# Kernel tuning notes

Hardware: AMD Instinct MI355X
Metric: run time of the kernel (lower is better)

Reference implementation:

```python
import jax, jax.numpy as jnp
import numpy as np

EPS = 1e-5

def _temporal_conv(x_bcnt, w, b):
    # x: (B,C,N,T), w: (O,I,1,K), pad time dim by K//2
    k = w.shape[-1]
    y = jax.lax.conv_general_dilated(
        x_bcnt, w, window_strides=(1, 1),
        padding=[(0, 0), (k // 2, k // 2)],
        dimension_numbers=("NCHW", "OIHW", "NCHW"))
    return y + b[None, :, None, None]

def _gcn(x_btnc, edge_index, w, b):
    # GCNConv: add self-loops, symmetric normalization, linear, scatter-add, bias.
    B, T, N, C = x_btnc.shape
    src = jnp.concatenate([edge_index[0], jnp.arange(N)])
    dst = jnp.concatenate([edge_index[1], jnp.arange(N)])
    ew = jnp.ones(src.shape[0], dtype=x_btnc.dtype)
    deg = jax.ops.segment_sum(ew, dst, num_segments=N)
    dinv = jnp.where(deg > 0, jax.lax.rsqrt(jnp.maximum(deg, 1e-12)), 0.0)
    norm = dinv[src] * dinv[dst] * ew  # (E+N,)
    xh = jnp.einsum("btnc,cd->btnd", x_btnc, w)
    msgs = xh[:, :, src, :] * norm[None, None, :, None]  # (B,T,E+N,C)
    agg = jnp.zeros_like(xh).at[:, :, dst, :].add(msgs)
    return agg + b

def _batchnorm2d(x_bcnt, gamma, beta):
    mean = jnp.mean(x_bcnt, axis=(0, 2, 3), keepdims=True)
    var = jnp.mean((x_bcnt - mean) ** 2, axis=(0, 2, 3), keepdims=True)
    xn = (x_bcnt - mean) * jax.lax.rsqrt(var + EPS)
    return xn * gamma[None, :, None, None] + beta[None, :, None, None]

def setup_inputs() -> dict:
    key = jax.random.key(0)
    ks = jax.random.split(key, 10)
    B, T, N, C = 1, 64, 2000, 64
    E, K = 32000, 3
    s = 1.0 / np.sqrt(C * K)
    inp = {
        "x": jax.random.normal(ks[0], (B, T, N, C), dtype=jnp.float32),
        "edge_index": jax.random.randint(ks[1], (2, E), 0, N, dtype=jnp.int64),
        "conv1_w": jax.random.uniform(ks[2], (C, C, 1, K), jnp.float32, -s, s),
        "conv1_b": jax.random.uniform(ks[3], (C,), jnp.float32, -s, s),
        "gcn_w": jax.random.normal(ks[4], (C, C), dtype=jnp.float32) / np.sqrt(C),
        "gcn_b": jnp.zeros((C,), dtype=jnp.float32),
        "conv2_w": jax.random.uniform(ks[5], (C, C, 1, K), jnp.float32, -s, s),
        "conv2_b": jax.random.uniform(ks[6], (C,), jnp.float32, -s, s),
        "bn_gamma": jnp.ones((C,), dtype=jnp.float32),
        "bn_beta": jnp.zeros((C,), dtype=jnp.float32),
    }
    return inp

def reference(x, edge_index, conv1_w, conv1_b, gcn_w, gcn_b, conv2_w, conv2_b, bn_gamma, bn_beta):
    # x: (B,T,N,C) -> (B,C,N,T)
    h = jnp.transpose(x, (0, 3, 2, 1))
    h = _temporal_conv(h, conv1_w, conv1_b)
    h = jnp.transpose(h, (0, 3, 2, 1))  # (B,T,N,C)
    h = _gcn(h, edge_index, gcn_w, gcn_b)
    h = jnp.transpose(h, (0, 3, 2, 1))  # (B,C,N,T)
    h = _temporal_conv(h, conv2_w, conv2_b)
    h = _batchnorm2d(h, bn_gamma, bn_beta)
    h = jax.nn.relu(h)
    return jnp.transpose(h, (0, 3, 2, 1))  # (B,T,N,C)
```

## Files before the change

kernel.cpp:

```cpp
#include <hip/hip_runtime.h>

#define T_DIM 64
#define N_DIM 2000
#define C_DIM 64
#define E_DIM 32000
#define ROWS (T_DIM * N_DIM)
#define BN_EPS 1e-5f
#define TCHUNK 4
#define UPN 2

typedef short s8v __attribute__((ext_vector_type(8)));
typedef float f4v __attribute__((ext_vector_type(4)));

__device__ __forceinline__ ushort f2b(float f) {
    unsigned u = __float_as_uint(f);
    unsigned r = u + 0x7FFF + ((u >> 16) & 1);
    return (ushort)(r >> 16);
}
__device__ __forceinline__ float b2f(ushort h) {
    return __uint_as_float(((unsigned)h) << 16);
}
__device__ __forceinline__ s8v pack8(float4 a, float4 b) {
    s8v r;
    r[0] = (short)f2b(a.x); r[1] = (short)f2b(a.y);
    r[2] = (short)f2b(a.z); r[3] = (short)f2b(a.w);
    r[4] = (short)f2b(b.x); r[5] = (short)f2b(b.y);
    r[6] = (short)f2b(b.z); r[7] = (short)f2b(b.w);
    return r;
}

__global__ void k_degscan(const int* __restrict__ ei, int* __restrict__ offs,
                          float* __restrict__ dinv, int* __restrict__ cursor,
                          int2* __restrict__ edat, float* __restrict__ bnstats) {
    __shared__ int a[2048], b[2048];
    int tid = threadIdx.x;
    for (int i = tid; i < 2048; i += 1024) a[i] = 0;
    __syncthreads();
    for (int e = tid; e < E_DIM; e += 1024) atomicAdd(&a[ei[E_DIM + e]], 1);
    __syncthreads();
    for (int i = tid; i < 2048; i += 1024) a[i] = (i < N_DIM) ? (a[i] + 1) : 0;
    __syncthreads();
    int* s = a; int* d = b;
    for (int off = 1; off < 2048; off <<= 1) {
        for (int i = tid; i < 2048; i += 1024)
            d[i] = s[i] + ((i >= off) ? s[i - off] : 0);
        __syncthreads();
        int* t = s; s = d; d = t;
    }
    for (int i = tid; i < 2048; i += 1024)
        if (i <= N_DIM) offs[i] = (i == 0) ? 0 : s[i - 1];
    for (int n = tid; n < N_DIM; n += 1024) {
        int pre = (n == 0) ? 0 : s[n - 1];
        int dp1 = s[n] - pre;
        float dn = rsqrtf((float)dp1);
        dinv[n] = dn;
        edat[pre] = make_int2(n, __float_as_int(dn * dn));
        cursor[n] = 1;
    }
    if (tid < 128) bnstats[tid] = 0.f;
}

__global__ __launch_bounds__(256) void k_fillw(
    const int* __restrict__ ei, const int* __restrict__ offs,
    const float* __restrict__ dinv, int* __restrict__ cursor,
    int2* __restrict__ edat,
    const float* __restrict__ c1w, const float* __restrict__ c1b,
    const float* __restrict__ gw, const float* __restrict__ gb,
    const float* __restrict__ c2b, const float* __restrict__ c2w,
    ushort* __restrict__ W5f, ushort* __restrict__ Wc,
    float* __restrict__ bz, float* __restrict__ beta) {
    int tid = threadIdx.x;
    if (blockIdx.x < 125) {
        int e = blockIdx.x * 256 + tid;
        if (e < E_DIM) {
            int s = ei[e];
            int d = ei[E_DIM + e];
            int p = atomicAdd(&cursor[d], 1);
            edat[offs[d] + p] = make_int2(s, __float_as_int(dinv[s] * dinv[d]));
        }
        return;
    }
    __shared__ float Gl[3][64];
    __shared__ float b1l[64], gbl[64];
    int i = blockIdx.x - 125;
    if (tid < 192) {
        int j = tid >> 6, c = tid & 63;
        float s = 0.f;
        for (int o = 0; o < 64; ++o)
            s += c1w[o * 192 + i * 3 + j] * gw[o * 64 + c];
        Gl[j][c] = s;
    } else {
        int c = tid - 192;
        float s = 0.f;
        if (i == 0)
            for (int o = 0; o < 64; ++o) s += c1b[o] * gw[o * 64 + c];
        b1l[c] = s;
        gbl[c] = gb[c];
    }
    __syncthreads();
    if (tid < 64) {
        int n = tid;
        float d00 = 0.f, d01 = 0.f, d02 = 0.f;
        float d10 = 0.f, d11 = 0.f, d12 = 0.f;
        float d20 = 0.f, d21 = 0.f, d22 = 0.f;
        for (int c = 0; c < 64; ++c) {
            float a0 = Gl[0][c], a1 = Gl[1][c], a2 = Gl[2][c];
            float b0 = c2w[n * 192 + c * 3 + 0];
            float b1 = c2w[n * 192 + c * 3 + 1];
            float b2 = c2w[n * 192 + c * 3 + 2];
            d00 += a0 * b0; d01 += a0 * b1; d02 += a0 * b2;
            d10 += a1 * b0; d11 += a1 * b1; d12 += a1 * b2;
            d20 += a2 * b0; d21 += a2 * b1; d22 += a2 * b2;
        }
        float wm[5];
        wm[0] = d00;
        wm[1] = d01 + d10;
        wm[2] = d02 + d11 + d20;
        wm[3] = d12 + d21;
        wm[4] = d22;
        for (int m = 0; m < 5; ++m) {
            int kk = m * 64 + i;
            int flat = (((kk >> 5) * 4 + (n >> 4)) * 64 + ((kk >> 3) & 3) * 16 + (n & 15)) * 8 + (kk & 7);
            W5f[flat] = f2b(wm[m]);
        }
        int fc = (((i >> 5) * 4 + (n >> 4)) * 64 + ((i >> 3) & 3) * 16 + (n & 15)) * 8 + (i & 7);
        Wc[fc] = f2b(-d20);
        Wc[4096 + fc] = f2b(-d02);
        if (i == 0) {
            float s1[3] = {0.f, 0.f, 0.f}, s2[3] = {0.f, 0.f, 0.f};
            for (int k = 0; k < 3; ++k)
                for (int c = 0; c < 64; ++c) {
                    float w2 = c2w[n * 192 + c * 3 + k];
                    s1[k] += b1l[c] * w2;
                    s2[k] += gbl[c] * w2;
                }
            bz[n]        = s1[0] + s1[1] + s1[2];
            bz[64 + n]   = s1[1] + s1[2];
            bz[128 + n]  = s1[0] + s1[1];
            float cb = c2b[n];
            beta[n]       = s2[0] + s2[1] + s2[2] + cb;
            beta[64 + n]  = s2[1] + s2[2] + cb;
            beta[128 + n] = s2[0] + s2[1] + cb;
        }
    }
}

__global__ __launch_bounds__(256) void k_conv5(
    const float* __restrict__ x, const ushort* __restrict__ W5f,
    const ushort* __restrict__ Wcg, const float* __restrict__ bz,
    ushort* __restrict__ z) {
    __shared__ __align__(16) ushort Wl[20480];
    __shared__ __align__(16) ushort Cl[4096];
    __shared__ __align__(16) ushort Eb[4][1280];

    int tid = threadIdx.x, wv = tid >> 6, lane = tid & 63;
    int ml = lane & 15, q = lane >> 4;
    int n0 = blockIdx.x * 64;
    int t0 = blockIdx.y * TCHUNK;
    int n = n0 + wv * 16 + ml;
    bool nok = (n < N_DIM);
    const float* xrow = x + (size_t)n * 64 + q * 8;

    #pragma unroll
    for (int o = 0; o < 10; ++o) {
        int idx = tid + o * 256;
        *(s8v*)&Wl[idx * 8] = *(const s8v*)&W5f[idx * 8];
    }
    bool bnd0 = (t0 == 0), bnd1 = (t0 + TCHUNK == T_DIM);
    if (bnd0 || bnd1) {
        const ushort* src = Wcg + (bnd1 ? 4096 : 0);
        #pragma unroll
        for (int o = 0; o < 2; ++o) {
            int idx = tid + o * 256;
            *(s8v*)&Cl[idx * 8] = *(const s8v*)&src[idx * 8];
        }
    }

    const s8v ZV = {0, 0, 0, 0, 0, 0, 0, 0};
    s8v a[16];
    #pragma unroll
    for (int i = 0; i < 16; ++i) a[i] = ZV;

    #pragma unroll
    for (int i = 0; i < 5; ++i) {
        int s = t0 - 2 + i;
        if (nok && s >= 0 && s < T_DIM) {
            const float* p = xrow + (size_t)s * N_DIM * 64;
            float4 v0 = *(const float4*)p;
            float4 v1 = *(const float4*)(p + 4);
            float4 v2 = *(const float4*)(p + 32);
            float4 v3 = *(const float4*)(p + 36);
            a[2 * i]     = pack8(v0, v1);
            a[2 * i + 1] = pack8(v2, v3);
        }
    }
    __syncthreads();

    #pragma unroll
    for (int p = 0; p < TCHUNK; ++p) {
        int t = t0 + p;
        float4 r0, r1, r2, r3;
        bool pf = false;
        if (p < TCHUNK - 1) {
            int s = t0 + 3 + p;
            if (nok && s < T_DIM) {
                pf = true;
                const float* pp = xrow + (size_t)s * N_DIM * 64;
                r0 = *(const float4*)pp;
                r1 = *(const float4*)(pp + 4);
                r2 = *(const float4*)(pp + 32);
                r3 = *(const float4*)(pp + 36);
            }
        }

        f4v acc[4];
        #pragma unroll
        for (int c = 0; c < 4; ++c) acc[c] = (f4v){0.f, 0.f, 0.f, 0.f};

        #pragma unroll
        for (int sg = 0; sg < 10; ++sg) {
            #pragma unroll
            for (int c = 0; c < 4; ++c) {
                s8v bf = *(const s8v*)&Wl[((sg * 4 + c) * 64 + lane) * 8];
                acc[c] = __builtin_amdgcn_mfma_f32_16x16x32_bf16(a[2 * p + sg], bf, acc[c], 0, 0, 0);
            }
        }
        if (bnd0 && p == 0) {
            #pragma unroll
            for (int s2 = 0; s2 < 2; ++s2)
                #pragma unroll
                for (int c = 0; c < 4; ++c) {
                    s8v bf = *(const s8v*)&Cl[((s2 * 4 + c) * 64 + lane) * 8];
                    acc[c] = __builtin_amdgcn_mfma_f32_16x16x32_bf16(a[4 + s2], bf, acc[c], 0, 0, 0);
                }
        }
        if (bnd1 && p == TCHUNK - 1) {
            #pragma unroll
            for (int s2 = 0; s2 < 2; ++s2)
                #pragma unroll
                for (int c = 0; c < 4; ++c) {
                    s8v bf = *(const s8v*)&Cl[((s2 * 4 + c) * 64 + lane) * 8];
                    acc[c] = __builtin_amdgcn_mfma_f32_16x16x32_bf16(a[10 + s2], bf, acc[c], 0, 0, 0);
                }
        }

        int cls = (bnd0 && p == 0) ? 1 : ((bnd1 && p == TCHUNK - 1) ? 2 : 0);
        ushort* eb = &Eb[wv][0];
        #pragma unroll
        for (int c = 0; c < 4; ++c) {
            int col = c * 16 + ml;
            float bb = bz[cls * 64 + col];
            #pragma unroll
            for (int rg = 0; rg < 4; ++rg)
                eb[(q * 4 + rg) * 80 + col] = f2b(acc[c][rg] + bb);
        }
        int rr = lane >> 2, cof = (lane & 3) * 16;
        int gn = n0 + wv * 16 + rr;
        if (gn < N_DIM) {
            ushort* dst = &z[((size_t)t * N_DIM + gn) * 64 + cof];
            *(s8v*)dst       = *(const s8v*)&eb[rr * 80 + cof];
            *(s8v*)(dst + 8) = *(const s8v*)&eb[rr * 80 + cof + 8];
        }
        if (p < TCHUNK - 1) {
            a[10 + 2 * p] = pf ? pack8(r0, r1) : ZV;
            a[11 + 2 * p] = pf ? pack8(r2, r3) : ZV;
        }
    }
}

__global__ __launch_bounds__(256) void k_gather(
    const ushort* __restrict__ zb, const int* __restrict__ offs,
    const int2* __restrict__ edat, const float* __restrict__ beta,
    ushort* __restrict__ yb, float* __restrict__ bnstats) {
    __shared__ float ssum[64], ssq[64];
    int tid = threadIdx.x;
    if (tid < 64) { ssum[tid] = 0.f; ssq[tid] = 0.f; }
    __syncthreads();

    int tg = blockIdx.x;
    int nb = blockIdx.y;
    int wv = tid >> 6, lane = tid & 63;
    int u = lane >> 3;
    int c8 = (lane & 7) * 8;
    int t = tg * 8 + u;
    int cls = (t == 0) ? 1 : ((t == 63) ? 2 : 0);
    const float* bp = beta + cls * 64 + c8;
    float4 b0 = *(const float4*)bp;
    float4 b1 = *(const float4*)(bp + 4);
    float bb[8] = {b0.x, b0.y, b0.z, b0.w, b1.x, b1.y, b1.z, b1.w};
    const ushort* zl = zb + (size_t)t * (N_DIM * 64) + c8;

    float sr[8] = {0.f,0.f,0.f,0.f,0.f,0.f,0.f,0.f};
    float qr[8] = {0.f,0.f,0.f,0.f,0.f,0.f,0.f,0.f};

    #pragma unroll
    for (int nn = 0; nn < UPN; ++nn) {
        int n = nb * (4 * UPN) + wv * UPN + nn;
        int beg = offs[n], end = offs[n + 1];

        float acc[8] = {0.f,0.f,0.f,0.f,0.f,0.f,0.f,0.f};
        int j = beg;
        for (; j + 1 < end; j += 2) {
            int2 e0 = edat[j];
            int2 e1 = edat[j + 1];
            float w0 = __int_as_float(e0.y);
            float w1 = __int_as_float(e1.y);
            s8v v0 = *(const s8v*)(zl + (size_t)e0.x * 64);
            s8v v1 = *(const s8v*)(zl + (size_t)e1.x * 64);
            #pragma unroll
            for (int i = 0; i < 8; ++i) acc[i] += w0 * b2f((ushort)v0[i]);
            #pragma unroll
            for (int i = 0; i < 8; ++i) acc[i] += w1 * b2f((ushort)v1[i]);
        }
        if (j < end) {
            int2 e0 = edat[j];
            float w0 = __int_as_float(e0.y);
            s8v v0 = *(const s8v*)(zl + (size_t)e0.x * 64);
            #pragma unroll
            for (int i = 0; i < 8; ++i) acc[i] += w0 * b2f((ushort)v0[i]);
        }

        s8v pk;
        #pragma unroll
        for (int i = 0; i < 8; ++i) {
            float y = acc[i] + bb[i];
            pk[i] = (short)f2b(y);
            sr[i] += y;
            qr[i] += y * y;
        }
        *(s8v*)&yb[((size_t)t * N_DIM + n) * 64 + c8] = pk;
    }

    #pragma unroll
    for (int dd = 8; dd <= 32; dd <<= 1)
        #pragma unroll
        for (int i = 0; i < 8; ++i) {
            sr[i] += __shfl_xor(sr[i], dd);
            qr[i] += __shfl_xor(qr[i], dd);
        }
    if (u == 0) {
        #pragma unroll
        for (int i = 0; i < 8; ++i) {
            atomicAdd(&ssum[c8 + i], sr[i]);
            atomicAdd(&ssq[c8 + i], qr[i]);
        }
    }
    __syncthreads();
    if (tid < 64) {
        atomicAdd(&bnstats[tid], ssum[tid]);
        atomicAdd(&bnstats[64 + tid], ssq[tid]);
    }
}

__global__ __launch_bounds__(256) void k_bn(const ushort* __restrict__ yb,
                                            const float* __restrict__ bnstats,
                                            const float* __restrict__ gamma,
                                            const float* __restrict__ beta,
                                            float* __restrict__ out) {
    __shared__ float sscale[64], sshift[64];
    int tid = threadIdx.x;
    if (tid < 64) {
        float m = bnstats[tid] * (1.0f / ROWS);
        float v = bnstats[64 + tid] * (1.0f / ROWS) - m * m;
        float sc = gamma[tid] * rsqrtf(v + BN_EPS);
        sscale[tid] = sc;
        sshift[tid] = beta[tid] - m * sc;
    }
    __syncthreads();
    const int total8 = ROWS * 8;
    for (int i8 = blockIdx.x * 256 + tid; i8 < total8; i8 += gridDim.x * 256) {
        s8v v = *(const s8v*)&yb[(size_t)i8 * 8];
        int c8 = (i8 & 7) * 8;
        f4v o0, o1;
        o0[0] = fmaxf(b2f((ushort)v[0]) * sscale[c8 + 0] + sshift[c8 + 0], 0.f);
        o0[1] = fmaxf(b2f((ushort)v[1]) * sscale[c8 + 1] + sshift[c8 + 1], 0.f);
        o0[2] = fmaxf(b2f((ushort)v[2]) * sscale[c8 + 2] + sshift[c8 + 2], 0.f);
        o0[3] = fmaxf(b2f((ushort)v[3]) * sscale[c8 + 3] + sshift[c8 + 3], 0.f);
        o1[0] = fmaxf(b2f((ushort)v[4]) * sscale[c8 + 4] + sshift[c8 + 4], 0.f);
        o1[1] = fmaxf(b2f((ushort)v[5]) * sscale[c8 + 5] + sshift[c8 + 5], 0.f);
        o1[2] = fmaxf(b2f((ushort)v[6]) * sscale[c8 + 6] + sshift[c8 + 6], 0.f);
        o1[3] = fmaxf(b2f((ushort)v[7]) * sscale[c8 + 7] + sshift[c8 + 7], 0.f);
        __builtin_nontemporal_store(o0, (f4v*)&out[(size_t)i8 * 8]);
        __builtin_nontemporal_store(o1, (f4v*)&out[(size_t)i8 * 8 + 4]);
    }
}

extern "C" void kernel_launch(void* const* d_in, const int* in_sizes, int n_in,
                              void* d_out, int out_size, void* d_ws, size_t ws_size,
                              hipStream_t stream) {
    const float* x   = (const float*)d_in[0];
    const int*   ei  = (const int*)d_in[1];
    const float* c1w = (const float*)d_in[2];
    const float* c1b = (const float*)d_in[3];
    const float* gw  = (const float*)d_in[4];
    const float* gb  = (const float*)d_in[5];
    const float* c2w = (const float*)d_in[6];
    const float* c2b = (const float*)d_in[7];
    const float* bng = (const float*)d_in[8];
    const float* bnb = (const float*)d_in[9];
    float* out = (float*)d_out;

    ushort* yb     = (ushort*)d_ws;
    ushort* W5f    = yb + (size_t)ROWS * 64;
    ushort* Wc     = W5f + 20480;
    float*  bz     = (float*)(Wc + 8192);
    float*  beta   = bz + 192;
    float*  dinv   = beta + 192;
    float*  bnstats= dinv + 2000;
    int*    offs   = (int*)(bnstats + 128);
    int*    cursor = offs + 2001;
    int2*   edat   = (int2*)((char*)(cursor + 2000) +
                     (((size_t)(cursor + 2000)) % 8 ? 4 : 0));

    ushort* zb = (ushort*)d_out;

    k_degscan<<<1, 1024, 0, stream>>>(ei, offs, dinv, cursor, edat, bnstats);
    k_fillw<<<189, 256, 0, stream>>>(ei, offs, dinv, cursor, edat,
                                     c1w, c1b, gw, gb, c2b, c2w, W5f, Wc, bz, beta);
    k_conv5<<<dim3(32, T_DIM / TCHUNK), 256, 0, stream>>>(x, W5f, Wc, bz, zb);
    k_gather<<<dim3(8, 250), 256, 0, stream>>>(zb, offs, edat, beta, yb, bnstats);
    k_bn<<<2048, 256, 0, stream>>>(yb, bnstats, bng, bnb, out);
}
```

Measured before the change: 211.7 us.

## Stage gather edge lists in LDS and unroll neighbor loads by eight

```diff
diff --git a/kernel.cpp b/kernel.cpp
--- a/kernel.cpp
+++ b/kernel.cpp
@@ -7,7 +7,7 @@
 #define ROWS (T_DIM * N_DIM)
 #define BN_EPS 1e-5f
 #define TCHUNK 4
-#define UPN 2
+#define GEMAX 1024
 
 typedef short s8v __attribute__((ext_vector_type(8)));
 typedef float f4v __attribute__((ext_vector_type(4)));
@@ -268,17 +268,28 @@
     }
 }
 
-__global__ __launch_bounds__(256) void k_gather(
+__global__ __launch_bounds__(512) void k_gather(
     const ushort* __restrict__ zb, const int* __restrict__ offs,
     const int2* __restrict__ edat, const float* __restrict__ beta,
     ushort* __restrict__ yb, float* __restrict__ bnstats) {
     __shared__ float ssum[64], ssq[64];
+    __shared__ int2 eLds[GEMAX];
+    __shared__ int eoff[9];
     int tid = threadIdx.x;
     if (tid < 64) { ssum[tid] = 0.f; ssq[tid] = 0.f; }
-    __syncthreads();
 
     int tg = blockIdx.x;
     int nb = blockIdx.y;
+    int n0 = nb * 8;
+    if (tid < 9) eoff[tid] = offs[n0 + tid];
+    __syncthreads();
+    int ebase = eoff[0];
+    int ecnt = eoff[8] - ebase;
+    bool inLds = (ecnt <= GEMAX);
+    if (inLds)
+        for (int i = tid; i < ecnt; i += 512) eLds[i] = edat[ebase + i];
+    __syncthreads();
+
     int wv = tid >> 6, lane = tid & 63;
     int u = lane >> 3;
     int c8 = (lane & 7) * 8;
@@ -290,46 +301,52 @@
     float bb[8] = {b0.x, b0.y, b0.z, b0.w, b1.x, b1.y, b1.z, b1.w};
     const ushort* zl = zb + (size_t)t * (N_DIM * 64) + c8;
 
-    float sr[8] = {0.f,0.f,0.f,0.f,0.f,0.f,0.f,0.f};
-    float qr[8] = {0.f,0.f,0.f,0.f,0.f,0.f,0.f,0.f};
-
-    #pragma unroll
-    for (int nn = 0; nn < UPN; ++nn) {
-        int n = nb * (4 * UPN) + wv * UPN + nn;
-        int beg = offs[n], end = offs[n + 1];
-
-        float acc[8] = {0.f,0.f,0.f,0.f,0.f,0.f,0.f,0.f};
-        int j = beg;
-        for (; j + 1 < end; j += 2) {
-            int2 e0 = edat[j];
-            int2 e1 = edat[j + 1];
-            float w0 = __int_as_float(e0.y);
-            float w1 = __int_as_float(e1.y);
-            s8v v0 = *(const s8v*)(zl + (size_t)e0.x * 64);
-            s8v v1 = *(const s8v*)(zl + (size_t)e1.x * 64);
-            #pragma unroll
-            for (int i = 0; i < 8; ++i) acc[i] += w0 * b2f((ushort)v0[i]);
-            #pragma unroll
-            for (int i = 0; i < 8; ++i) acc[i] += w1 * b2f((ushort)v1[i]);
-        }
-        if (j < end) {
-            int2 e0 = edat[j];
-            float w0 = __int_as_float(e0.y);
-            s8v v0 = *(const s8v*)(zl + (size_t)e0.x * 64);
-            #pragma unroll
-            for (int i = 0; i < 8; ++i) acc[i] += w0 * b2f((ushort)v0[i]);
-        }
-
-        s8v pk;
-        #pragma unroll
-        for (int i = 0; i < 8; ++i) {
-            float y = acc[i] + bb[i];
-            pk[i] = (short)f2b(y);
-            sr[i] += y;
-            qr[i] += y * y;
-        }
-        *(s8v*)&yb[((size_t)t * N_DIM + n) * 64 + c8] = pk;
-    }
+    int n = n0 + wv;
+    int beg = eoff[wv] - ebase;
+    int len = eoff[wv + 1] - ebase - beg;
+
+    float acc[8] = {0.f,0.f,0.f,0.f,0.f,0.f,0.f,0.f};
+
+    if (inLds) {
+        for (int k = 0; k < len; k += 8) {
+            int2 e[8];
+            #pragma unroll
+            for (int i = 0; i < 8; ++i) {
+                int kk = k + i;
+                e[i] = eLds[beg + (kk < len ? kk : 0)];
+            }
+            s8v v[8];
+            #pragma unroll
+            for (int i = 0; i < 8; ++i)
+                v[i] = *(const s8v*)(zl + (size_t)e[i].x * 64);
+            #pragma unroll
+            for (int i = 0; i < 8; ++i) {
+                float w = (k + i < len) ? __int_as_float(e[i].y) : 0.f;
+                #pragma unroll
+                for (int j = 0; j < 8; ++j) acc[j] += w * b2f((ushort)v[i][j]);
+            }
+        }
+    } else {
+        const int2* eg = edat + ebase;
+        for (int k = 0; k < len; ++k) {
+            int2 e = eg[beg + k];
+            float w = __int_as_float(e.y);
+            s8v v = *(const s8v*)(zl + (size_t)e.x * 64);
+            #pragma unroll
+            for (int i = 0; i < 8; ++i) acc[i] += w * b2f((ushort)v[i]);
+        }
+    }
+
+    float sr[8], qr[8];
+    s8v pk;
+    #pragma unroll
+    for (int i = 0; i < 8; ++i) {
+        float y = acc[i] + bb[i];
+        pk[i] = (short)f2b(y);
+        sr[i] = y;
+        qr[i] = y * y;
+    }
+    *(s8v*)&yb[((size_t)t * N_DIM + n) * 64 + c8] = pk;
 
     #pragma unroll
     for (int dd = 8; dd <= 32; dd <<= 1)
@@ -418,6 +435,6 @@
     k_fillw<<<189, 256, 0, stream>>>(ei, offs, dinv, cursor, edat,
                                      c1w, c1b, gw, gb, c2b, c2w, W5f, Wc, bz, beta);
     k_conv5<<<dim3(32, T_DIM / TCHUNK), 256, 0, stream>>>(x, W5f, Wc, bz, zb);
-    k_gather<<<dim3(8, 250), 256, 0, stream>>>(zb, offs, edat, beta, yb, bnstats);
+    k_gather<<<dim3(8, 250), 512, 0, stream>>>(zb, offs, edat, beta, yb, bnstats);
     k_bn<<<2048, 256, 0, stream>>>(yb, bnstats, bng, bnb, out);
 }
```

New measurement: 205.1 us. 1.03x faster.
